# Optimization experiments

Measured on AMD Instinct MI355X. Metric: run time of the kernel, lower is better.

## Reference

```python
import jax, jax.numpy as jnp
import numpy as np
import math

NB_STEPS = 50          # quadrature sub-intervals -> 51 Clenshaw-Curtis points
NUM_RNN_STEPS = 2


def _cc_weights(nb_steps):
    # Faithful port of UMNN's compute_cc_weights (Clenshaw-Curtis quadrature).
    lam = np.arange(0, nb_steps + 1).reshape(-1, 1).astype(np.float64)
    lam = np.cos((lam @ lam.T) * math.pi / nb_steps)
    lam[:, 0] = 0.5
    lam[:, -1] = 0.5 * lam[:, -1]
    lam = lam * 2.0 / nb_steps
    W = np.arange(0, nb_steps + 1).reshape(-1, 1).astype(np.float64)
    W[np.arange(1, nb_steps + 1, 2)] = 0
    W = 2.0 / (1.0 - W ** 2)
    W[0] = 1.0
    W[np.arange(1, nb_steps + 1, 2)] = 0
    cc = (lam.T @ W).astype(np.float32).reshape(-1)                      # [S]
    steps = np.cos(np.arange(0, nb_steps + 1) * math.pi / nb_steps).astype(np.float32)  # [S]
    return jnp.asarray(cc), jnp.asarray(steps)

CC_W, CC_STEPS = _cc_weights(NB_STEPS)  # S = NB_STEPS + 1 = 51


def _integrand(t, h, W1, b1, W2, b2, W3, b3, final_w):
    # IntegrandNN: MLP(cat(t,h)) -> ELU + 1 (>=0) -> fused power features -> ReLU(Linear)
    z = jnp.concatenate([t, h], axis=1)          # [N, in_d]
    z = jax.nn.relu(z @ W1.T + b1)               # [N, 128]
    z = jax.nn.relu(z @ W2.T + b2)               # [N, 128]
    z = jax.nn.elu(z @ W3.T + b3) + 1.0          # [N, 1], >= 0
    p = jnp.concatenate([z ** 1.5, z ** 2, z ** 2.5, z ** 3, z ** 3.5], axis=1)  # [N, 5]
    return jax.nn.relu((1.0 / (p + 1.0)) @ final_w.T)  # [N, 1]


def _inner_integral(x, h, params):
    # InnerUMNN: integral of IntegrandNN from x to xmax, xmax = max(x) + 10 (global scalar)
    N = x.shape[0]
    S = NB_STEPS + 1
    xmax = jnp.max(x) + 10.0
    T = x + (xmax - x) * (CC_STEPS[None, :] + 1.0) * 0.5   # [N, S]
    Tf = T.reshape(N * S, 1)
    hf = jnp.broadcast_to(h[:, None, :], (N, S, h.shape[1])).reshape(N * S, -1)
    g = _integrand(Tf, hf, *params).reshape(N, S)
    z = jnp.sum(g * CC_W[None, :], axis=1, keepdims=True)  # [N, 1]
    return z * (xmax - x) * 0.5


def _outer_integral(xT, h, params):
    # ParallelNeuralIntegral of InnerUMNN from x0 = 0 to xT; xT: [B, 1]
    B = xT.shape[0]
    S = NB_STEPS + 1
    X = xT * (CC_STEPS[None, :] + 1.0) * 0.5               # [B, S] (x0 = 0)
    Xf = X.reshape(B * S, 1)
    hf = jnp.broadcast_to(h[:, None, :], (B, S, h.shape[1])).reshape(B * S, -1)
    f = _inner_integral(Xf, hf, params).reshape(B, S)      # nested quadrature
    z = jnp.sum(f * CC_W[None, :], axis=1, keepdims=True)  # [B, 1]
    return z * xT * 0.5


def setup_inputs() -> dict:
    key = jax.random.key(0)
    ks = jax.random.split(key, 8)
    B, NF, IN_D, H = 256, 512, 64, 128
    x_ = jax.random.normal(ks[0], (B, NF), jnp.float32)
    h_ = jax.random.normal(ks[1], (B, IN_D - 1), jnp.float32)

    def lin(k, o, i):
        lim = 1.0 / np.sqrt(i)
        kw, kb = jax.random.split(k)
        return (jax.random.uniform(kw, (o, i), jnp.float32, -lim, lim),
                jax.random.uniform(kb, (o,), jnp.float32, -lim, lim))

    W1, b1 = lin(ks[2], H, IN_D)
    W2, b2 = lin(ks[3], H, H)
    W3, b3 = lin(ks[4], 1, H)
    lim5 = 1.0 / np.sqrt(5.0)
    final_w = jnp.abs(jax.random.uniform(ks[5], (1, 5), jnp.float32, -lim5, lim5))  # reset_params: abs
    log_weight = jnp.ones((1, NF), jnp.float32)            # reset_parameters: all ones
    sigmoid_param = jax.random.normal(ks[6], (1,), jnp.float32)
    return dict(x_=x_, h_=h_, W1=W1, b1=b1, W2=W2, b2=b2, W3=W3, b3=b3,
                final_w=final_w, log_weight=log_weight, sigmoid_param=sigmoid_param)


def reference(x_, h_, W1, b1, W2, b2, W3, b3, final_w, log_weight, sigmoid_param):
    params = (W1, b1, W2, b2, W3, b3, final_w)
    # compute_modular_function: F.linear then sum over dim 1 -> [B, 1]
    xm = jnp.sum(x_ @ log_weight.T, axis=1, keepdims=True)
    lam = jax.nn.sigmoid(sigmoid_param)                    # [1]
    out = jnp.zeros_like(xm)
    for _ in range(NUM_RNN_STEPS):
        xT = (1.0 - lam) * xm + lam * out
        out = _outer_integral(xT, h_, params)
    return out
```

## Files before the change

kernel.cpp:

```cpp
#include <hip/hip_runtime.h>
#include <math.h>

#define BB 256
#define NF 512
#define IND 64
#define HD 128
#define SS 51
#define NHM1 63

#define WS_LAM  0
#define WS_CCW  16
#define WS_U    80
#define WS_XM   144
#define WS_OUT1 656
#define WSH_C1  2048
#define WSH_W1  34816
#define WSH_W2F 40960

typedef _Float16 f16x2 __attribute__((ext_vector_type(2)));
typedef __fp16   fp16x2 __attribute__((ext_vector_type(2)));
typedef _Float16 f16x8 __attribute__((ext_vector_type(8)));
typedef float    f32x16 __attribute__((ext_vector_type(16)));

union f16x8_split { f16x8 v8; f16x2 v2[4]; };
union pk_cast { fp16x2 p; f16x2 f; };

static __device__ inline f16x2 cvt_pk(float a, float b) {
    pk_cast u; u.p = __builtin_amdgcn_cvt_pkrtz(a, b);
    return u.f;
}

static __device__ inline float dot2f(f16x2 a, f16x2 b, float c) {
#if __has_builtin(__builtin_amdgcn_fdot2)
    return __builtin_amdgcn_fdot2(a, b, c, false);
#else
    return c + (float)a[0] * (float)b[0] + (float)a[1] * (float)b[1];
#endif
}

__global__ void k_setup(const float* __restrict__ x_, const float* __restrict__ h_,
                        const float* __restrict__ W1, const float* __restrict__ b1,
                        const float* __restrict__ W2, const float* __restrict__ lw,
                        const float* __restrict__ sp, float* __restrict__ ws) {
    int b = blockIdx.x;
    int j = threadIdx.x;
    short* wsh = (short*)ws;

    float acc = b1[j];
    const float* w1row = W1 + j * IND;
    const float* hrow  = h_ + b * NHM1;
    #pragma unroll 7
    for (int k = 0; k < NHM1; ++k) acc = fmaf(w1row[1 + k], hrow[k], acc);
    {
        _Float16 hv = (_Float16)acc;
        short sv; __builtin_memcpy(&sv, &hv, 2);
        wsh[WSH_C1 + b * HD + j] = sv;
    }

    float s = 0.f;
    for (int k = j; k < NF; k += HD) s = fmaf(x_[b * NF + k], lw[k], s);
    __shared__ float red[HD];
    red[j] = s;
    __syncthreads();
    for (int off = 64; off > 0; off >>= 1) {
        if (j < off) red[j] += red[j + off];
        __syncthreads();
    }
    if (j == 0) ws[WS_XM + b] = red[0];

    if (b < 128) {
        int d = b * 128 + j;
        int i = d & 7, lane = (d >> 3) & 63, kn = d >> 9;
        int kk = kn >> 2, nt = kn & 3;
        int row = nt * 32 + (lane & 31);
        int k = kk * 16 + (lane >> 5) * 8 + i;
        _Float16 hv = (_Float16)W2[row * HD + k];
        short sv; __builtin_memcpy(&sv, &hv, 2);
        wsh[WSH_W2F + d] = sv;
    }

    if (b == 0) {
        if (j < SS) {
            float acc2 = 0.f;
            for (int jj = 0; jj <= 50; jj += 2) {
                float wj = (jj == 0) ? 1.f : 2.f / (1.f - (float)(jj * jj));
                float lamv;
                if (j == 0 || j == 50) {
                    lamv = 0.02f;
                } else {
                    int m = (jj * j) % 100;
                    lamv = cosf((float)m * (float)M_PI / 50.f) * 0.04f;
                }
                acc2 = fmaf(lamv, wj, acc2);
            }
            ws[WS_CCW + j] = acc2;
            float st = cosf((float)j * (float)M_PI / 50.f);
            ws[WS_U + j] = (st + 1.f) * 0.5f;
        }
        if (j == 127) ws[WS_LAM] = 1.f / (1.f + expf(-sp[0]));
    }
    if (b == 2) {
        _Float16 hv = (_Float16)W1[j * IND];
        short sv; __builtin_memcpy(&sv, &hv, 2);
        wsh[WSH_W1 + j] = sv;
    }
    if (b == 4) ws[WS_OUT1 + j] = 0.f;
    if (b == 5) ws[WS_OUT1 + 128 + j] = 0.f;
}

__launch_bounds__(256, 2)
__global__ void k_int(const float* __restrict__ b2, const float* __restrict__ W3,
                      const float* __restrict__ b3, const float* __restrict__ fw,
                      const float* __restrict__ ws, const float* __restrict__ outprev,
                      float* __restrict__ tgt, float* __restrict__ ztgt) {
    int b = blockIdx.x >> 1, hf = blockIdx.x & 1;
    int tid = threadIdx.x;
    int wv = tid >> 6, l = tid & 63;
    int e32 = l & 31, h2 = l >> 5;
    int pi = wv & 1, ps = wv >> 1;

    __shared__ float us[SS], ccs[SS], xw[4];
    __shared__ short c1h[HD], w1h[HD];
    __shared__ float part[2][2][2][32];

    if (ztgt && hf == 0 && tid == 0) ztgt[b] = 0.f;
    if (tid < SS) { us[tid] = ws[WS_U + tid]; ccs[tid] = ws[WS_CCW + tid]; }
    {
        const short* wsh0 = (const short*)ws;
        if (tid < HD) { c1h[tid] = wsh0[WSH_C1 + b * HD + tid]; w1h[tid] = wsh0[WSH_W1 + tid]; }
    }

    float lam = ws[WS_LAM];
    float xmv = ws[WS_XM + tid];
    float opv = outprev ? outprev[tid] : 0.f;
    float xtv = (1.f - lam) * xmv + lam * opv;
    float mx = fmaxf(xtv, 0.f);
    #pragma unroll
    for (int off = 32; off >= 1; off >>= 1) mx = fmaxf(mx, __shfl_xor(mx, off, 64));
    if (l == 0) xw[wv] = mx;
    __syncthreads();
    float xmax = fmaxf(fmaxf(xw[0], xw[1]), fmaxf(xw[2], xw[3])) + 10.f;
    float xT = (1.f - lam) * ws[WS_XM + b] + lam * (outprev ? outprev[b] : 0.f);

    const short* wsh = (const short*)ws;

    f16x8 Af[8][2];
    #pragma unroll
    for (int kk = 0; kk < 8; ++kk)
        #pragma unroll
        for (int u = 0; u < 2; ++u) {
            int ntg = 2 * pi + u;
            Af[kk][u] = *reinterpret_cast<const f16x8*>(
                wsh + WSH_W2F + ((kk * 4 + ntg) * 64 + l) * 8);
        }

    f16x2 b2pk[2][8], w3pk[2][8];
    #pragma unroll
    for (int u = 0; u < 2; ++u) {
        int jb = (2 * pi + u) * 32;
        #pragma unroll
        for (int q = 0; q < 8; ++q) {
            int r0 = ((2 * q) & 3) + 8 * ((2 * q) >> 2) + 4 * h2;
            b2pk[u][q] = cvt_pk(b2[jb + r0], b2[jb + r0 + 1]);
            w3pk[u][q] = cvt_pk(W3[jb + r0], W3[jb + r0 + 1]);
        }
    }
    float b3v = b3[0];
    float fw0 = fw[0], fw1 = fw[1], fw2 = fw[2], fw3 = fw[3], fw4 = fw[4];

    float accO = 0.f;
    float zs_prev = 0.f, w_prev = 0.f;
    int buf = 0;
    const f16x2 z2 = {(_Float16)0.f, (_Float16)0.f};

    #pragma unroll 1
    for (int it = 0; it < 21; ++it) {
        int tl = hf * 42 + ps * 21 + it;
        int m = tl * 32 + e32;
        int valid = (m <= 2600);
        int mm = valid ? m : 2600;
        int s  = (mm * 41121) >> 21;
        int si = mm - s * 51;
        float x = xT * us[s];
        float range = xmax - x;
        float t = fmaf(range, us[si], x);
        float wgt = valid ? (ccs[si] * ccs[s] * range * xT * 0.25f) : 0.f;
        float wsel = (h2 == 0 && (e32 >> 4) == pi) ? wgt : 0.f;
        _Float16 th = (_Float16)t;
        f16x2 tv = {th, th};

        f32x16 C0, C1;
        #pragma unroll
        for (int e = 0; e < 16; ++e) { C0[e] = 0.f; C1[e] = 0.f; }

        {
            float z = zs_prev > 0.f ? zs_prev + 1.f : __expf(zs_prev);
            float sq = sqrtf(z);
            float p15 = z * sq, p2 = z * z, p25 = p2 * sq, p3 = p2 * z, p35 = p3 * sq;
            float g = fw0 * __builtin_amdgcn_rcpf(p15 + 1.f)
                    + fw1 * __builtin_amdgcn_rcpf(p2  + 1.f)
                    + fw2 * __builtin_amdgcn_rcpf(p25 + 1.f)
                    + fw3 * __builtin_amdgcn_rcpf(p3  + 1.f)
                    + fw4 * __builtin_amdgcn_rcpf(p35 + 1.f);
            g = fmaxf(g, 0.f);
            accO = fmaf(g, w_prev, accO);
        }

        #pragma unroll
        for (int kk = 0; kk < 8; ++kk) {
            f16x8_split c8, w8, Bu;
            c8.v8 = *reinterpret_cast<const f16x8*>(&c1h[kk * 16 + h2 * 8]);
            w8.v8 = *reinterpret_cast<const f16x8*>(&w1h[kk * 16 + h2 * 8]);
            #pragma unroll
            for (int p = 0; p < 4; ++p)
                Bu.v2[p] = __builtin_elementwise_max(
                    __builtin_elementwise_fma(w8.v2[p], tv, c8.v2[p]), z2);
            C0 = __builtin_amdgcn_mfma_f32_32x32x16_f16(Af[kk][0], Bu.v8, C0, 0, 0, 0);
            C1 = __builtin_amdgcn_mfma_f32_32x32x16_f16(Af[kk][1], Bu.v8, C1, 0, 0, 0);
        }

        float za = 0.f, zb = 0.f;
        #pragma unroll
        for (int q = 0; q < 8; ++q) {
            f16x2 a0 = cvt_pk(C0[2 * q], C0[2 * q + 1]);
            a0 = __builtin_elementwise_max(a0 + b2pk[0][q], z2);
            za = dot2f(a0, w3pk[0][q], za);
            f16x2 a1 = cvt_pk(C1[2 * q], C1[2 * q + 1]);
            a1 = __builtin_elementwise_max(a1 + b2pk[1][q], z2);
            zb = dot2f(a1, w3pk[1][q], zb);
        }
        float zhalf = za + zb;
        zhalf += __shfl_xor(zhalf, 32, 64);
        if (h2 == 0) part[ps][pi][buf][e32] = zhalf;
        __syncthreads();
        float zoth = part[ps][pi ^ 1][buf][e32];
        zs_prev = zhalf + zoth + b3v;
        w_prev = wsel;
        buf ^= 1;
    }

    {
        float z = zs_prev > 0.f ? zs_prev + 1.f : __expf(zs_prev);
        float sq = sqrtf(z);
        float p15 = z * sq, p2 = z * z, p25 = p2 * sq, p3 = p2 * z, p35 = p3 * sq;
        float g = fw0 * __builtin_amdgcn_rcpf(p15 + 1.f)
                + fw1 * __builtin_amdgcn_rcpf(p2  + 1.f)
                + fw2 * __builtin_amdgcn_rcpf(p25 + 1.f)
                + fw3 * __builtin_amdgcn_rcpf(p3  + 1.f)
                + fw4 * __builtin_amdgcn_rcpf(p35 + 1.f);
        g = fmaxf(g, 0.f);
        accO = fmaf(g, w_prev, accO);
    }

    #pragma unroll
    for (int off = 32; off >= 1; off >>= 1) accO += __shfl_xor(accO, off, 64);
    if (l == 0) atomicAdd(&tgt[b], accO);
}

extern "C" void kernel_launch(void* const* d_in, const int* in_sizes, int n_in,
                              void* d_out, int out_size, void* d_ws, size_t ws_size,
                              hipStream_t stream) {
    (void)in_sizes; (void)n_in; (void)out_size; (void)ws_size;
    const float* x_ = (const float*)d_in[0];
    const float* h_ = (const float*)d_in[1];
    const float* W1 = (const float*)d_in[2];
    const float* b1 = (const float*)d_in[3];
    const float* W2 = (const float*)d_in[4];
    const float* b2 = (const float*)d_in[5];
    const float* W3 = (const float*)d_in[6];
    const float* b3 = (const float*)d_in[7];
    const float* fw = (const float*)d_in[8];
    const float* lw = (const float*)d_in[9];
    const float* sp = (const float*)d_in[10];
    float* wsf  = (float*)d_ws;
    float* out1 = wsf + WS_OUT1;
    float* out  = (float*)d_out;

    k_setup<<<BB, HD, 0, stream>>>(x_, h_, W1, b1, W2, lw, sp, wsf);
    k_int<<<BB * 2, 256, 0, stream>>>(b2, W3, b3, fw, wsf, nullptr, out1, out);
    k_int<<<BB * 2, 256, 0, stream>>>(b2, W3, b3, fw, wsf, out1, out, nullptr);
}
```

Before: 81.46 us.

## Stage W2 in LDS so each wave computes full hidden dim without block sync

Before, each wave held half of the W2 fragments in registers and two waves split the 128 hidden outputs, exchanging partial sums through shared memory with a __syncthreads every iteration. Now the whole W2 fragment array is copied into LDS and every wave computes all four 32-row tiles itself, reading A operands from LDS. This removes the per-iteration barrier and cross-wave exchange, and spreads point tiles round-robin across waves (11 iterations instead of 21). It costs 32KB of LDS per block, which may limit occupancy, plus LDS read traffic on every MFMA. Sched barriers are added to control how the LDS loads interleave with the MFMAs.

```diff
diff --git a/kernel.cpp b/kernel.cpp
--- a/kernel.cpp
+++ b/kernel.cpp
@@ -16,6 +16,7 @@
 #define WSH_C1  2048
 #define WSH_W1  34816
 #define WSH_W2F 40960
+#define WS_W2F_F4 5120
 
 typedef _Float16 f16x2 __attribute__((ext_vector_type(2)));
 typedef __fp16   fp16x2 __attribute__((ext_vector_type(2)));
@@ -117,18 +118,24 @@
     int tid = threadIdx.x;
     int wv = tid >> 6, l = tid & 63;
     int e32 = l & 31, h2 = l >> 5;
-    int pi = wv & 1, ps = wv >> 1;
-
+
+    __shared__ __align__(16) short w2s[16384];
+    __shared__ __align__(16) short c1h[HD], w1h[HD];
     __shared__ float us[SS], ccs[SS], xw[4];
-    __shared__ short c1h[HD], w1h[HD];
-    __shared__ float part[2][2][2][32];
 
     if (ztgt && hf == 0 && tid == 0) ztgt[b] = 0.f;
-    if (tid < SS) { us[tid] = ws[WS_U + tid]; ccs[tid] = ws[WS_CCW + tid]; }
+
+    {
+        const float4* src = reinterpret_cast<const float4*>(ws) + WS_W2F_F4;
+        float4* dst = reinterpret_cast<float4*>(w2s);
+        #pragma unroll
+        for (int k = 0; k < 8; ++k) dst[tid + k * 256] = src[tid + k * 256];
+    }
     {
         const short* wsh0 = (const short*)ws;
         if (tid < HD) { c1h[tid] = wsh0[WSH_C1 + b * HD + tid]; w1h[tid] = wsh0[WSH_W1 + tid]; }
     }
+    if (tid < SS) { us[tid] = ws[WS_U + tid]; ccs[tid] = ws[WS_CCW + tid]; }
 
     float lam = ws[WS_LAM];
     float xmv = ws[WS_XM + tid];
@@ -142,27 +149,15 @@
     float xmax = fmaxf(fmaxf(xw[0], xw[1]), fmaxf(xw[2], xw[3])) + 10.f;
     float xT = (1.f - lam) * ws[WS_XM + b] + lam * (outprev ? outprev[b] : 0.f);
 
-    const short* wsh = (const short*)ws;
-
-    f16x8 Af[8][2];
+    f16x2 b2pk[4][8], w3pk[4][8];
     #pragma unroll
-    for (int kk = 0; kk < 8; ++kk)
-        #pragma unroll
-        for (int u = 0; u < 2; ++u) {
-            int ntg = 2 * pi + u;
-            Af[kk][u] = *reinterpret_cast<const f16x8*>(
-                wsh + WSH_W2F + ((kk * 4 + ntg) * 64 + l) * 8);
-        }
-
-    f16x2 b2pk[2][8], w3pk[2][8];
-    #pragma unroll
-    for (int u = 0; u < 2; ++u) {
-        int jb = (2 * pi + u) * 32;
+    for (int nt = 0; nt < 4; ++nt) {
+        int jb = nt * 32;
         #pragma unroll
         for (int q = 0; q < 8; ++q) {
             int r0 = ((2 * q) & 3) + 8 * ((2 * q) >> 2) + 4 * h2;
-            b2pk[u][q] = cvt_pk(b2[jb + r0], b2[jb + r0 + 1]);
-            w3pk[u][q] = cvt_pk(W3[jb + r0], W3[jb + r0 + 1]);
+            b2pk[nt][q] = cvt_pk(b2[jb + r0], b2[jb + r0 + 1]);
+            w3pk[nt][q] = cvt_pk(W3[jb + r0], W3[jb + r0 + 1]);
         }
     }
     float b3v = b3[0];
@@ -170,12 +165,11 @@
 
     float accO = 0.f;
     float zs_prev = 0.f, w_prev = 0.f;
-    int buf = 0;
     const f16x2 z2 = {(_Float16)0.f, (_Float16)0.f};
 
     #pragma unroll 1
-    for (int it = 0; it < 21; ++it) {
-        int tl = hf * 42 + ps * 21 + it;
+    for (int it = 0; it < 11; ++it) {
+        int tl = hf * 4 + wv + it * 8;
         int m = tl * 32 + e32;
         int valid = (m <= 2600);
         int mm = valid ? m : 2600;
@@ -185,13 +179,13 @@
         float range = xmax - x;
         float t = fmaf(range, us[si], x);
         float wgt = valid ? (ccs[si] * ccs[s] * range * xT * 0.25f) : 0.f;
-        float wsel = (h2 == 0 && (e32 >> 4) == pi) ? wgt : 0.f;
+        float wsel = h2 ? 0.f : wgt;
         _Float16 th = (_Float16)t;
         f16x2 tv = {th, th};
 
-        f32x16 C0, C1;
-        #pragma unroll
-        for (int e = 0; e < 16; ++e) { C0[e] = 0.f; C1[e] = 0.f; }
+        f32x16 C0, C1, C2, C3;
+        #pragma unroll
+        for (int e = 0; e < 16; ++e) { C0[e] = 0.f; C1[e] = 0.f; C2[e] = 0.f; C3[e] = 0.f; }
 
         {
             float z = zs_prev > 0.f ? zs_prev + 1.f : __expf(zs_prev);
@@ -207,19 +201,29 @@
         }
 
         #pragma unroll
-        for (int kk = 0; kk < 8; ++kk) {
-            f16x8_split c8, w8, Bu;
-            c8.v8 = *reinterpret_cast<const f16x8*>(&c1h[kk * 16 + h2 * 8]);
-            w8.v8 = *reinterpret_cast<const f16x8*>(&w1h[kk * 16 + h2 * 8]);
+        for (int kp = 0; kp < 4; ++kp) {
+            __builtin_amdgcn_sched_barrier(0);
             #pragma unroll
-            for (int p = 0; p < 4; ++p)
-                Bu.v2[p] = __builtin_elementwise_max(
-                    __builtin_elementwise_fma(w8.v2[p], tv, c8.v2[p]), z2);
-            C0 = __builtin_amdgcn_mfma_f32_32x32x16_f16(Af[kk][0], Bu.v8, C0, 0, 0, 0);
-            C1 = __builtin_amdgcn_mfma_f32_32x32x16_f16(Af[kk][1], Bu.v8, C1, 0, 0, 0);
-        }
-
-        float za = 0.f, zb = 0.f;
+            for (int kd = 0; kd < 2; ++kd) {
+                int kk = kp * 2 + kd;
+                f16x8_split c8, w8, Bu;
+                c8.v8 = *reinterpret_cast<const f16x8*>(&c1h[kk * 16 + h2 * 8]);
+                w8.v8 = *reinterpret_cast<const f16x8*>(&w1h[kk * 16 + h2 * 8]);
+                #pragma unroll
+                for (int p = 0; p < 4; ++p)
+                    Bu.v2[p] = __builtin_elementwise_max(
+                        __builtin_elementwise_fma(w8.v2[p], tv, c8.v2[p]), z2);
+                const f16x8* Afp = reinterpret_cast<const f16x8*>(
+                    &w2s[(kk * 4 * 64 + l) * 8]);
+                C0 = __builtin_amdgcn_mfma_f32_32x32x16_f16(Afp[ 0], Bu.v8, C0, 0, 0, 0);
+                C1 = __builtin_amdgcn_mfma_f32_32x32x16_f16(Afp[ 64], Bu.v8, C1, 0, 0, 0);
+                C2 = __builtin_amdgcn_mfma_f32_32x32x16_f16(Afp[128], Bu.v8, C2, 0, 0, 0);
+                C3 = __builtin_amdgcn_mfma_f32_32x32x16_f16(Afp[192], Bu.v8, C3, 0, 0, 0);
+            }
+        }
+        __builtin_amdgcn_sched_barrier(0);
+
+        float za = 0.f, zb = 0.f, zc = 0.f, zd = 0.f;
         #pragma unroll
         for (int q = 0; q < 8; ++q) {
             f16x2 a0 = cvt_pk(C0[2 * q], C0[2 * q + 1]);
@@ -228,15 +232,17 @@
             f16x2 a1 = cvt_pk(C1[2 * q], C1[2 * q + 1]);
             a1 = __builtin_elementwise_max(a1 + b2pk[1][q], z2);
             zb = dot2f(a1, w3pk[1][q], zb);
-        }
-        float zhalf = za + zb;
-        zhalf += __shfl_xor(zhalf, 32, 64);
-        if (h2 == 0) part[ps][pi][buf][e32] = zhalf;
-        __syncthreads();
-        float zoth = part[ps][pi ^ 1][buf][e32];
-        zs_prev = zhalf + zoth + b3v;
+            f16x2 a2 = cvt_pk(C2[2 * q], C2[2 * q + 1]);
+            a2 = __builtin_elementwise_max(a2 + b2pk[2][q], z2);
+            zc = dot2f(a2, w3pk[2][q], zc);
+            f16x2 a3 = cvt_pk(C3[2 * q], C3[2 * q + 1]);
+            a3 = __builtin_elementwise_max(a3 + b2pk[3][q], z2);
+            zd = dot2f(a3, w3pk[3][q], zd);
+        }
+        float z1 = (za + zb) + (zc + zd);
+        z1 += __shfl_xor(z1, 32, 64);
+        zs_prev = z1 + b3v;
         w_prev = wsel;
-        buf ^= 1;
     }
 
     {
```

After: 75.66 us. 1.08x faster.
